# Kernel tuning notes

Measured on AMD Instinct MI355X. Metric: run time of the kernel, lower is better.

Reference implementation:

```python
import jax, jax.numpy as jnp
import numpy as np

H = 16       # num_attention_heads
KV = 4       # num_key_value_heads
HD = 128     # head_dim
BASE = 10000.0


def rotate_half(x):
    x1, x2 = jnp.split(x, 2, axis=-1)
    return jnp.concatenate((-x2, x1), axis=-1)


def rope_cos_sin(position_ids):
    # inv_freq: (HD/2,)
    inv_freq = 1.0 / (BASE ** (jnp.arange(0, HD, 2, dtype=jnp.float32) / HD))
    freqs = position_ids.astype(jnp.float32)[..., None] * inv_freq  # (B, S, HD/2)
    emb = jnp.concatenate((freqs, freqs), axis=-1)  # (B, S, HD)
    return jnp.cos(emb), jnp.sin(emb)


def setup_inputs() -> dict:
    key = jax.random.key(0)
    ks = jax.random.split(key, 5)
    B, S, D = 2, 2048, 2048
    sc = 1.0 / np.sqrt(D)
    return {
        "hidden_states": jax.random.normal(ks[0], (B, S, D), jnp.float32),
        "position_ids": jnp.broadcast_to(jnp.arange(S, dtype=jnp.int32), (B, S)),
        "wq": jax.random.normal(ks[1], (H * HD, D), jnp.float32) * sc,
        "wk": jax.random.normal(ks[2], (KV * HD, D), jnp.float32) * sc,
        "wv": jax.random.normal(ks[3], (KV * HD, D), jnp.float32) * sc,
        "wo": jax.random.normal(ks[4], (H * HD, H * HD), jnp.float32) * sc,
    }


def attention_forward(hidden_states, position_ids, wq, wk, wv, wo):
    B, S, D = hidden_states.shape
    n_rep = H // KV
    # projections -> (B, heads, S, HD)
    q = (hidden_states @ wq.T).reshape(B, S, H, HD).transpose(0, 2, 1, 3)
    k = (hidden_states @ wk.T).reshape(B, S, KV, HD).transpose(0, 2, 1, 3)
    v = (hidden_states @ wv.T).reshape(B, S, KV, HD).transpose(0, 2, 1, 3)
    # RoPE
    cos, sin = rope_cos_sin(position_ids)  # (B, S, HD)
    cos = cos[:, None]  # (B, 1, S, HD)
    sin = sin[:, None]
    q = q * cos + rotate_half(q) * sin
    k = k * cos + rotate_half(k) * sin
    # repeat kv heads for GQA: (B, KV, S, HD) -> (B, H, S, HD)
    k = jnp.repeat(k, n_rep, axis=1)
    v = jnp.repeat(v, n_rep, axis=1)
    scale = 1.0 / np.sqrt(HD)
    scores = jnp.einsum("bhqd,bhkd->bhqk", q, k) * scale
    attn = jax.nn.softmax(scores.astype(jnp.float32), axis=-1).astype(q.dtype)
    out = jnp.einsum("bhqk,bhkd->bhqd", attn, v)
    out = out.transpose(0, 2, 1, 3).reshape(B, S, H * HD)
    return out @ wo.T


def reference(hidden_states, position_ids, wq, wk, wv, wo):
    return attention_forward(hidden_states, position_ids, wq, wk, wv, wo)
```

## Files before the change

kernel.cpp:

```cpp
#include <hip/hip_runtime.h>
#include <hip/hip_bf16.h>
#include <math.h>


typedef __attribute__((ext_vector_type(4))) float f32x4;
typedef __attribute__((ext_vector_type(8))) short short8;
typedef __attribute__((ext_vector_type(4))) unsigned short u16x4;
typedef __attribute__((ext_vector_type(8))) unsigned short u16x8;

static __device__ __forceinline__ unsigned short f2bf(float x) {
    unsigned u = __builtin_bit_cast(unsigned, x);
    u += 0x7fffu + ((u >> 16) & 1u);
    return (unsigned short)(u >> 16);
}
static __device__ __forceinline__ float bf2f(unsigned short h) {
    unsigned u = ((unsigned)h) << 16;
    return __builtin_bit_cast(float, u);
}

static __device__ __forceinline__ void gload16(const unsigned short* g, unsigned short* lds) {
    __builtin_amdgcn_global_load_lds((const __attribute__((address_space(1))) void*)g,
                                     (__attribute__((address_space(3))) void*)lds, 16, 0, 0);
}

__global__ __launch_bounds__(256) void k_conv(const float* __restrict__ src,
                                              unsigned short* __restrict__ dst, int n4) {
    int i = blockIdx.x * 256 + threadIdx.x;
    if (i >= n4) return;
    f32x4 v = ((const f32x4*)src)[i];
    u16x4 o;
    o.x = f2bf(v.x); o.y = f2bf(v.y); o.z = f2bf(v.z); o.w = f2bf(v.w);
    ((u16x4*)dst)[i] = o;
}

__global__ __launch_bounds__(256) void k_conv_wqkv(const float* __restrict__ wq,
                                                   const float* __restrict__ wk,
                                                   const float* __restrict__ wv,
                                                   unsigned short* __restrict__ dst) {
    int i = blockIdx.x * 256 + threadIdx.x;
    long flat = (long)i * 4;
    int row = (int)(flat >> 11);
    int col = (int)(flat & 2047);
    const float* src;
    if (row < 2048)      src = wq + (size_t)row * 2048;
    else if (row < 2560) src = wk + (size_t)(row - 2048) * 2048;
    else                 src = wv + (size_t)(row - 2560) * 2048;
    f32x4 v = *(const f32x4*)(src + col);
    u16x4 o;
    o.x = f2bf(v.x); o.y = f2bf(v.y); o.z = f2bf(v.z); o.w = f2bf(v.w);
    *(u16x4*)(dst + flat) = o;
}

__global__ void k_rope_table(const int* __restrict__ pos_ids, float2* __restrict__ tb) {
    int r = blockIdx.x;
    int i = threadIdx.x;
    float pos = (float)pos_ids[r];
    float powv = (float)pow(10000.0, (double)i / 64.0);
    float invf = 1.0f / powv;
    float arg  = pos * invf;
    double a = (double)arg;
    tb[(size_t)r * 64 + i] = make_float2((float)cos(a), (float)sin(a));
}

__global__ __launch_bounds__(256) void k_rope_apply(unsigned short* __restrict__ qkv,
                                                    const float2* __restrict__ tb) {
    int row = blockIdx.x;
    int tid = threadIdx.x;
    int dp = tid & 63;
    float2 cs = tb[(size_t)row * 64 + dp];
    size_t base = (size_t)row * 3072;
    const float qs = 0.08838834764831845f;
    #pragma unroll
    for (int j = tid; j < 1024; j += 256) {
        int h = j >> 6;
        size_t off = base + h * 128 + dp;
        float x0 = bf2f(qkv[off]), x1 = bf2f(qkv[off + 64]);
        qkv[off]      = f2bf((x0 * cs.x - x1 * cs.y) * qs);
        qkv[off + 64] = f2bf((x1 * cs.x + x0 * cs.y) * qs);
    }
    {
        int kv = tid >> 6;
        size_t off = base + 2048 + kv * 128 + dp;
        float x0 = bf2f(qkv[off]), x1 = bf2f(qkv[off + 64]);
        qkv[off]      = f2bf(x0 * cs.x - x1 * cs.y);
        qkv[off + 64] = f2bf(x1 * cs.x + x0 * cs.y);
    }
}

__global__ __launch_bounds__(256) void k_vtrans(const unsigned short* __restrict__ qkv,
                                                unsigned short* __restrict__ vt) {
    int idx = blockIdx.x * 256 + threadIdx.x;
    int schunk = idx & 255;
    int orow = idx >> 8;
    int d = orow & 127;
    int bkv = orow >> 7;
    int b = bkv >> 2, kv = bkv & 3;
    const unsigned short* src = qkv + (size_t)(b * 2048 + schunk * 8) * 3072 + 2560 + kv * 128 + d;
    u16x8 v;
    #pragma unroll
    for (int j = 0; j < 8; ++j) v[j] = src[(size_t)j * 3072];
    *(u16x8*)(vt + (size_t)orow * 2048 + schunk * 8) = v;
}

template <int OUTF32>
__global__ __launch_bounds__(256) void k_gemm_bt(const unsigned short* __restrict__ A,
                                                 const unsigned short* __restrict__ W,
                                                 void* __restrict__ Cout,
                                                 int M, int N, int K) {
    __shared__ unsigned short As[4096];
    __shared__ unsigned short Ws[4096];
    const int tid = threadIdx.x;
    const int lane = tid & 63;
    const int w = tid >> 6;
    const int q = lane & 15, g = lane >> 4;
    const int wr = w >> 1, wc = w & 1;
    const long mbase = (long)blockIdx.y * 128;
    const long nbase = (long)blockIdx.x * 128;

    const unsigned short* gA[2];
    const unsigned short* gW[2];
    #pragma unroll
    for (int j = 0; j < 2; ++j) {
        int r = j * 64 + (tid >> 2);
        int slot = (tid & 3) ^ ((r >> 1) & 3);
        gA[j] = A + (size_t)(mbase + r) * K + slot * 8;
        gW[j] = W + (size_t)(nbase + r) * K + slot * 8;
    }
    const int sa = (g ^ ((q >> 1) & 3)) * 8;

    f32x4 acc[4][4];
    #pragma unroll
    for (int m = 0; m < 4; ++m)
        #pragma unroll
        for (int n = 0; n < 4; ++n) acc[m][n] = (f32x4){0.f, 0.f, 0.f, 0.f};

    for (int kk = 0; kk < K; kk += 32) {
        __syncthreads();
        #pragma unroll
        for (int j = 0; j < 2; ++j) {
            gload16(gA[j], &As[j * 2048 + w * 512]);
            gload16(gW[j], &Ws[j * 2048 + w * 512]);
            gA[j] += 32; gW[j] += 32;
        }
        __syncthreads();
        short8 af[4], bfr[4];
        #pragma unroll
        for (int m = 0; m < 4; ++m) af[m] = *(const short8*)&As[(wr * 64 + m * 16 + q) * 32 + sa];
        #pragma unroll
        for (int n = 0; n < 4; ++n) bfr[n] = *(const short8*)&Ws[(wc * 64 + n * 16 + q) * 32 + sa];
        #pragma unroll
        for (int m = 0; m < 4; ++m)
            #pragma unroll
            for (int n = 0; n < 4; ++n)
                acc[m][n] = __builtin_amdgcn_mfma_f32_16x16x32_bf16(af[m], bfr[n], acc[m][n], 0, 0, 0);
    }

    #pragma unroll
    for (int m = 0; m < 4; ++m)
        #pragma unroll
        for (int n = 0; n < 4; ++n)
            #pragma unroll
            for (int rr = 0; rr < 4; ++rr) {
                long row = mbase + wr * 64 + m * 16 + 4 * g + rr;
                long col = nbase + wc * 64 + n * 16 + q;
                if (OUTF32) ((float*)Cout)[row * N + col] = acc[m][n][rr];
                else ((unsigned short*)Cout)[row * N + col] = f2bf(acc[m][n][rr]);
            }
}

__global__ __launch_bounds__(256, 2) void k_flash(const unsigned short* __restrict__ qkv,
                                                  const unsigned short* __restrict__ vt,
                                                  unsigned short* __restrict__ aout) {
    __shared__ unsigned short Ks[2][8192];
    __shared__ unsigned short Vs[2][8192];
    __shared__ unsigned short Plds[4][1152];
    const int wg = blockIdx.x;
    const int kvg = wg & 7;
    const int inner = wg >> 3;
    const int h_in = inner & 3;
    const int qt = inner >> 2;
    const int b = kvg >> 2, kvh = kvg & 3;
    const int h = kvh * 4 + h_in;
    const int tid = threadIdx.x;
    const int w = tid >> 6, lane = tid & 63;
    const int q = lane & 15, g = lane >> 4;
    const int qrow = qt * 128 + w * 32;

    short8 qf[2][4];
    #pragma unroll
    for (int u = 0; u < 2; ++u) {
        const unsigned short* Qp = qkv + (size_t)(b * 2048 + qrow + u * 16 + q) * 3072 + h * 128 + g * 8;
        #pragma unroll
        for (int t = 0; t < 4; ++t) qf[u][t] = *(const short8*)(Qp + t * 32);
    }

    const unsigned short* Kbase = qkv + (size_t)(b * 2048) * 3072 + 2048 + kvh * 128;
    const unsigned short* Vbase = vt + (size_t)((b * 4 + kvh) * 128) * 2048;
    const unsigned short* gK[4];
    const unsigned short* gV[4];
    #pragma unroll
    for (int i = 0; i < 4; ++i) {
        int rowK = w * 16 + i * 4 + (lane >> 4);
        gK[i] = Kbase + (size_t)rowK * 3072 + (((lane & 15) ^ (rowK & 7)) << 3);
        int rowV = w * 32 + i * 8 + (lane >> 3);
        gV[i] = Vbase + (size_t)rowV * 2048 + (((lane & 7) ^ (rowV & 7)) << 3);
    }

    const int swz = (q & 7) << 3;
    int tcK[4];
    #pragma unroll
    for (int t = 0; t < 4; ++t) tcK[t] = (t * 32 + g * 8) ^ swz;

    unsigned short* Pw = Plds[w];

    float m_run[2] = {-INFINITY, -INFINITY};
    float l_run[2] = {0.f, 0.f};
    f32x4 o[2][8];
    #pragma unroll
    for (int u = 0; u < 2; ++u)
        #pragma unroll
        for (int nf = 0; nf < 8; ++nf) o[u][nf] = (f32x4){0.f, 0.f, 0.f, 0.f};

    auto STAGE = [&](int buf) {
        #pragma unroll
        for (int i = 0; i < 4; ++i) {
            gload16(gK[i], &Ks[buf][w * 2048 + i * 512]);
            gload16(gV[i], &Vs[buf][w * 2048 + i * 512]);
            gK[i] += 64 * 3072;
            gV[i] += 64;
        }
    };

    STAGE(0);
    int cur = 0;
    for (int t0 = 0; t0 < 32; ++t0) {
        if (t0 > 0) __builtin_amdgcn_s_barrier();
        if (t0 + 1 < 32) {
            STAGE(cur ^ 1);
            asm volatile("s_waitcnt vmcnt(8)" ::: "memory");
        } else {
            asm volatile("s_waitcnt vmcnt(0)" ::: "memory");
        }
        __builtin_amdgcn_s_barrier();

        const unsigned short* Kt = Ks[cur];
        const unsigned short* Vt = Vs[cur];

        f32x4 st[2][4];
        #pragma unroll
        for (int ks = 0; ks < 4; ++ks) {
            f32x4 a0 = (f32x4){0.f, 0.f, 0.f, 0.f};
            f32x4 a1 = (f32x4){0.f, 0.f, 0.f, 0.f};
            int rb = (ks * 16 + q) * 128;
            #pragma unroll
            for (int t = 0; t < 4; ++t) {
                short8 kf = *(const short8*)&Kt[rb + tcK[t]];
                a0 = __builtin_amdgcn_mfma_f32_16x16x32_bf16(kf, qf[0][t], a0, 0, 0, 0);
                a1 = __builtin_amdgcn_mfma_f32_16x16x32_bf16(kf, qf[1][t], a1, 0, 0, 0);
            }
            st[0][ks] = a0; st[1][ks] = a1;
        }

        short8 pa[2][2];
        #pragma unroll
        for (int u = 0; u < 2; ++u) {
            float mx = -INFINITY;
            #pragma unroll
            for (int ks = 0; ks < 4; ++ks)
                #pragma unroll
                for (int rr = 0; rr < 4; ++rr) mx = fmaxf(mx, st[u][ks][rr]);
            mx = fmaxf(mx, __shfl_xor(mx, 16));
            mx = fmaxf(mx, __shfl_xor(mx, 32));
            if (__any(mx - m_run[u] > 8.0f)) {
                float mn = fmaxf(m_run[u], mx);
                float sc = __expf(m_run[u] - mn);
                l_run[u] *= sc;
                f32x4 sv;
                #pragma unroll
                for (int rr = 0; rr < 4; ++rr) sv[rr] = __shfl(sc, 4 * g + rr);
                #pragma unroll
                for (int nf = 0; nf < 8; ++nf) o[u][nf] *= sv;
                m_run[u] = mn;
            }
            float ls = 0.f;
            float p[4][4];
            #pragma unroll
            for (int ks = 0; ks < 4; ++ks)
                #pragma unroll
                for (int rr = 0; rr < 4; ++rr) {
                    float pv = __expf(st[u][ks][rr] - m_run[u]);
                    p[ks][rr] = pv; ls += pv;
                }
            ls += __shfl_xor(ls, 16);
            ls += __shfl_xor(ls, 32);
            l_run[u] += ls;

            #pragma unroll
            for (int ks = 0; ks < 4; ++ks) {
                u16x4 pk;
                #pragma unroll
                for (int rr = 0; rr < 4; ++rr) pk[rr] = f2bf(p[ks][rr]);
                *(u16x4*)&Pw[q * 72 + ks * 16 + 4 * g] = pk;
            }
            asm volatile("s_waitcnt lgkmcnt(0)" ::: "memory");
            pa[u][0] = *(const short8*)&Pw[q * 72 + g * 8];
            pa[u][1] = *(const short8*)&Pw[q * 72 + 32 + g * 8];
        }

        #pragma unroll
        for (int nf = 0; nf < 8; ++nf) {
            int rb = (nf * 16 + q) * 64;
            f32x4 b0 = o[0][nf], b1 = o[1][nf];
            #pragma unroll
            for (int t = 0; t < 2; ++t) {
                short8 vf = *(const short8*)&Vt[rb + tcK[t]];
                b0 = __builtin_amdgcn_mfma_f32_16x16x32_bf16(pa[0][t], vf, b0, 0, 0, 0);
                b1 = __builtin_amdgcn_mfma_f32_16x16x32_bf16(pa[1][t], vf, b1, 0, 0, 0);
            }
            o[0][nf] = b0; o[1][nf] = b1;
        }
        cur ^= 1;
    }

    #pragma unroll
    for (int u = 0; u < 2; ++u) {
        f32x4 li;
        #pragma unroll
        for (int rr = 0; rr < 4; ++rr) li[rr] = __shfl(l_run[u], 4 * g + rr);
        #pragma unroll
        for (int nf = 0; nf < 8; ++nf)
            #pragma unroll
            for (int rr = 0; rr < 4; ++rr) {
                size_t row = (size_t)(b * 2048 + qrow + u * 16 + 4 * g + rr);
                aout[row * 2048 + h * 128 + nf * 16 + q] = f2bf(o[u][nf][rr] / li[rr]);
            }
    }
}

extern "C" void kernel_launch(void* const* d_in, const int* in_sizes, int n_in,
                              void* d_out, int out_size, void* d_ws, size_t ws_size,
                              hipStream_t stream) {
    (void)in_sizes; (void)n_in; (void)out_size; (void)ws_size;
    const float* hs = (const float*)d_in[0];
    const int* pos  = (const int*)d_in[1];
    const float* wq = (const float*)d_in[2];
    const float* wk = (const float*)d_in[3];
    const float* wv = (const float*)d_in[4];
    const float* wo = (const float*)d_in[5];
    float* out = (float*)d_out;

    unsigned short* hsb   = (unsigned short*)d_ws;
    unsigned short* wqkvb = hsb + (size_t)4096 * 2048;
    unsigned short* wob   = wqkvb + (size_t)3072 * 2048;
    unsigned short* qkvt  = wob + (size_t)2048 * 2048;
    unsigned short* vtb   = qkvt + (size_t)4096 * 3072;
    float2* tb            = (float2*)(vtb + (size_t)8 * 128 * 2048);
    unsigned short* aoutb = (unsigned short*)(tb + (size_t)4096 * 64);

    k_conv<<<8192, 256, 0, stream>>>(hs, hsb, 2097152);
    k_conv_wqkv<<<6144, 256, 0, stream>>>(wq, wk, wv, wqkvb);
    k_conv<<<4096, 256, 0, stream>>>(wo, wob, 1048576);
    k_rope_table<<<4096, 64, 0, stream>>>(pos, tb);
    k_gemm_bt<0><<<dim3(24, 32), 256, 0, stream>>>(hsb, wqkvb, (void*)qkvt, 4096, 3072, 2048);
    k_rope_apply<<<4096, 256, 0, stream>>>(qkvt, tb);
    k_vtrans<<<1024, 256, 0, stream>>>(qkvt, vtb);
    k_flash<<<dim3(512), 256, 0, stream>>>(qkvt, vtb, aoutb);
    k_gemm_bt<1><<<dim3(16, 32), 256, 0, stream>>>(aoutb, wob, (void*)out, 4096, 2048, 2048);
}
```

Before: 258.7 us.

## Fuse RoPE and V transpose into QKV GEMM epilogue, double-buffer GEMM, use exp2

The Q and K weight rows are permuted at conversion time so that each RoPE pair lands in adjacent output columns. That lets the QKV GEMM epilogue apply RoPE with a lane shuffle, fold in the softmax scale times log2(e), and write V straight into transposed layout. This removes the separate rope_apply and vtrans kernels and their extra passes over the QKV buffer. The GEMM main loop gains LDS double buffering with explicit vmcnt waits. The flash kernel switches from __expf to raw v_exp_f32 and preloads the V fragments before the softmax; this raises register pressure and moves work into a more complex epilogue with strided stores.

```diff
diff --git a/kernel.cpp b/kernel.cpp
--- a/kernel.cpp
+++ b/kernel.cpp
@@ -17,7 +17,11 @@
     unsigned u = ((unsigned)h) << 16;
     return __builtin_bit_cast(float, u);
 }
-
+static __device__ __forceinline__ float exp2_fast(float x) {
+    float r;
+    asm volatile("v_exp_f32 %0, %1" : "=v"(r) : "v"(x));
+    return r;
+}
 static __device__ __forceinline__ void gload16(const unsigned short* g, unsigned short* lds) {
     __builtin_amdgcn_global_load_lds((const __attribute__((address_space(1))) void*)g,
                                      (__attribute__((address_space(3))) void*)lds, 16, 0, 0);
@@ -42,9 +46,14 @@
     int row = (int)(flat >> 11);
     int col = (int)(flat & 2047);
     const float* src;
-    if (row < 2048)      src = wq + (size_t)row * 2048;
-    else if (row < 2560) src = wk + (size_t)(row - 2048) * 2048;
-    else                 src = wv + (size_t)(row - 2560) * 2048;
+    if (row < 2560) {
+        int base = row & 2047;
+        int hh = base >> 7, ii = base & 127;
+        int d = (ii >> 1) + ((ii & 1) << 6);
+        src = (row < 2048 ? wq : wk) + (size_t)(hh * 128 + d) * 2048;
+    } else {
+        src = wv + (size_t)(row - 2560) * 2048;
+    }
     f32x4 v = *(const f32x4*)(src + col);
     u16x4 o;
     o.x = f2bf(v.x); o.y = f2bf(v.y); o.z = f2bf(v.z); o.w = f2bf(v.w);
@@ -62,53 +71,16 @@
     tb[(size_t)r * 64 + i] = make_float2((float)cos(a), (float)sin(a));
 }
 
-__global__ __launch_bounds__(256) void k_rope_apply(unsigned short* __restrict__ qkv,
-                                                    const float2* __restrict__ tb) {
-    int row = blockIdx.x;
-    int tid = threadIdx.x;
-    int dp = tid & 63;
-    float2 cs = tb[(size_t)row * 64 + dp];
-    size_t base = (size_t)row * 3072;
-    const float qs = 0.08838834764831845f;
-    #pragma unroll
-    for (int j = tid; j < 1024; j += 256) {
-        int h = j >> 6;
-        size_t off = base + h * 128 + dp;
-        float x0 = bf2f(qkv[off]), x1 = bf2f(qkv[off + 64]);
-        qkv[off]      = f2bf((x0 * cs.x - x1 * cs.y) * qs);
-        qkv[off + 64] = f2bf((x1 * cs.x + x0 * cs.y) * qs);
-    }
-    {
-        int kv = tid >> 6;
-        size_t off = base + 2048 + kv * 128 + dp;
-        float x0 = bf2f(qkv[off]), x1 = bf2f(qkv[off + 64]);
-        qkv[off]      = f2bf(x0 * cs.x - x1 * cs.y);
-        qkv[off + 64] = f2bf(x1 * cs.x + x0 * cs.y);
-    }
-}
-
-__global__ __launch_bounds__(256) void k_vtrans(const unsigned short* __restrict__ qkv,
-                                                unsigned short* __restrict__ vt) {
-    int idx = blockIdx.x * 256 + threadIdx.x;
-    int schunk = idx & 255;
-    int orow = idx >> 8;
-    int d = orow & 127;
-    int bkv = orow >> 7;
-    int b = bkv >> 2, kv = bkv & 3;
-    const unsigned short* src = qkv + (size_t)(b * 2048 + schunk * 8) * 3072 + 2560 + kv * 128 + d;
-    u16x8 v;
-    #pragma unroll
-    for (int j = 0; j < 8; ++j) v[j] = src[(size_t)j * 3072];
-    *(u16x8*)(vt + (size_t)orow * 2048 + schunk * 8) = v;
-}
-
-template <int OUTF32>
-__global__ __launch_bounds__(256) void k_gemm_bt(const unsigned short* __restrict__ A,
-                                                 const unsigned short* __restrict__ W,
-                                                 void* __restrict__ Cout,
-                                                 int M, int N, int K) {
-    __shared__ unsigned short As[4096];
-    __shared__ unsigned short Ws[4096];
+template <int EPI>
+__global__ __launch_bounds__(256) void k_gemm(const unsigned short* __restrict__ A,
+                                              const unsigned short* __restrict__ W,
+                                              float* __restrict__ Cf,
+                                              unsigned short* __restrict__ qkvt,
+                                              unsigned short* __restrict__ vtb,
+                                              const float2* __restrict__ tb,
+                                              int M, int N, int K) {
+    __shared__ unsigned short As[2][4096];
+    __shared__ unsigned short Ws[2][4096];
     const int tid = threadIdx.x;
     const int lane = tid & 63;
     const int w = tid >> 6;
@@ -134,38 +106,91 @@
         #pragma unroll
         for (int n = 0; n < 4; ++n) acc[m][n] = (f32x4){0.f, 0.f, 0.f, 0.f};
 
-    for (int kk = 0; kk < K; kk += 32) {
-        __syncthreads();
+    auto STAGE = [&](int buf) {
         #pragma unroll
         for (int j = 0; j < 2; ++j) {
-            gload16(gA[j], &As[j * 2048 + w * 512]);
-            gload16(gW[j], &Ws[j * 2048 + w * 512]);
+            gload16(gA[j], &As[buf][j * 2048 + w * 512]);
+            gload16(gW[j], &Ws[buf][j * 2048 + w * 512]);
             gA[j] += 32; gW[j] += 32;
         }
-        __syncthreads();
+    };
+
+    const int nk = K >> 5;
+    STAGE(0);
+    int cur = 0;
+    for (int t = 0; t < nk; ++t) {
+        if (t) __builtin_amdgcn_s_barrier();
+        if (t + 1 < nk) {
+            STAGE(cur ^ 1);
+            asm volatile("s_waitcnt vmcnt(4)" ::: "memory");
+        } else {
+            asm volatile("s_waitcnt vmcnt(0)" ::: "memory");
+        }
+        __builtin_amdgcn_s_barrier();
+
         short8 af[4], bfr[4];
         #pragma unroll
-        for (int m = 0; m < 4; ++m) af[m] = *(const short8*)&As[(wr * 64 + m * 16 + q) * 32 + sa];
-        #pragma unroll
-        for (int n = 0; n < 4; ++n) bfr[n] = *(const short8*)&Ws[(wc * 64 + n * 16 + q) * 32 + sa];
+        for (int m = 0; m < 4; ++m) af[m] = *(const short8*)&As[cur][(wr * 64 + m * 16 + q) * 32 + sa];
+        #pragma unroll
+        for (int n = 0; n < 4; ++n) bfr[n] = *(const short8*)&Ws[cur][(wc * 64 + n * 16 + q) * 32 + sa];
         #pragma unroll
         for (int m = 0; m < 4; ++m)
             #pragma unroll
             for (int n = 0; n < 4; ++n)
                 acc[m][n] = __builtin_amdgcn_mfma_f32_16x16x32_bf16(af[m], bfr[n], acc[m][n], 0, 0, 0);
-    }
-
-    #pragma unroll
-    for (int m = 0; m < 4; ++m)
-        #pragma unroll
-        for (int n = 0; n < 4; ++n)
-            #pragma unroll
-            for (int rr = 0; rr < 4; ++rr) {
-                long row = mbase + wr * 64 + m * 16 + 4 * g + rr;
-                long col = nbase + wc * 64 + n * 16 + q;
-                if (OUTF32) ((float*)Cout)[row * N + col] = acc[m][n][rr];
-                else ((unsigned short*)Cout)[row * N + col] = f2bf(acc[m][n][rr]);
-            }
+        cur ^= 1;
+    }
+
+    if (EPI == 0) {
+        #pragma unroll
+        for (int m = 0; m < 4; ++m)
+            #pragma unroll
+            for (int n = 0; n < 4; ++n)
+                #pragma unroll
+                for (int rr = 0; rr < 4; ++rr) {
+                    long row = mbase + wr * 64 + m * 16 + 4 * g + rr;
+                    long col = nbase + wc * 64 + n * 16 + q;
+                    Cf[row * N + col] = acc[m][n][rr];
+                }
+    } else {
+        const int tile = blockIdx.x;
+        if (tile >= 20) {
+            const int kv = tile - 20;
+            #pragma unroll
+            for (int m = 0; m < 4; ++m)
+                #pragma unroll
+                for (int n = 0; n < 4; ++n) {
+                    int c = wc * 64 + n * 16 + q;
+                    long r0 = mbase + wr * 64 + m * 16 + 4 * g;
+                    int b = (int)(r0 >> 11), s0 = (int)(r0 & 2047);
+                    u16x4 pk;
+                    #pragma unroll
+                    for (int rr = 0; rr < 4; ++rr) pk[rr] = f2bf(acc[m][n][rr]);
+                    *(u16x4*)(vtb + (size_t)((b * 4 + kv) * 128 + c) * 2048 + s0) = pk;
+                }
+        } else {
+            const float scale = (tile < 16) ? 0.12751744f : 1.0f;
+            const float sgn = (q & 1) ? 1.f : -1.f;
+            #pragma unroll
+            for (int m = 0; m < 4; ++m)
+                #pragma unroll
+                for (int rr = 0; rr < 4; ++rr) {
+                    long row = mbase + wr * 64 + m * 16 + 4 * g + rr;
+                    #pragma unroll
+                    for (int n = 0; n < 4; ++n) {
+                        int c = wc * 64 + n * 16 + q;
+                        float x = acc[m][n][rr];
+                        float p = __shfl_xor(x, 1);
+                        float2 cs = tb[row * 64 + (c >> 1)];
+                        float y = (x * cs.x + sgn * (p * cs.y)) * scale;
+                        int dorig = (c >> 1) + ((c & 1) << 6);
+                        long col = (tile < 16) ? (tile * 128 + dorig)
+                                               : (2048 + (tile - 16) * 128 + dorig);
+                        qkvt[row * 3072 + col] = f2bf(y);
+                    }
+                }
+        }
+    }
 }
 
 __global__ __launch_bounds__(256, 2) void k_flash(const unsigned short* __restrict__ qkv,
@@ -261,19 +286,26 @@
             st[0][ks] = a0; st[1][ks] = a1;
         }
 
-        short8 pa[2][2];
+        short8 vf[8][2];
+        #pragma unroll
+        for (int nf = 0; nf < 8; ++nf) {
+            int rb = (nf * 16 + q) * 64;
+            #pragma unroll
+            for (int t = 0; t < 2; ++t) vf[nf][t] = *(const short8*)&Vt[rb + tcK[t]];
+        }
+
         #pragma unroll
         for (int u = 0; u < 2; ++u) {
-            float mx = -INFINITY;
-            #pragma unroll
-            for (int ks = 0; ks < 4; ++ks)
-                #pragma unroll
-                for (int rr = 0; rr < 4; ++rr) mx = fmaxf(mx, st[u][ks][rr]);
+            float mx = fmaxf(
+                fmaxf(fmaxf(fmaxf(st[u][0][0], st[u][0][1]), fmaxf(st[u][0][2], st[u][0][3])),
+                      fmaxf(fmaxf(st[u][1][0], st[u][1][1]), fmaxf(st[u][1][2], st[u][1][3]))),
+                fmaxf(fmaxf(fmaxf(st[u][2][0], st[u][2][1]), fmaxf(st[u][2][2], st[u][2][3])),
+                      fmaxf(fmaxf(st[u][3][0], st[u][3][1]), fmaxf(st[u][3][2], st[u][3][3]))));
             mx = fmaxf(mx, __shfl_xor(mx, 16));
             mx = fmaxf(mx, __shfl_xor(mx, 32));
             if (__any(mx - m_run[u] > 8.0f)) {
                 float mn = fmaxf(m_run[u], mx);
-                float sc = __expf(m_run[u] - mn);
+                float sc = exp2_fast(m_run[u] - mn);
                 l_run[u] *= sc;
                 f32x4 sv;
                 #pragma unroll
@@ -282,15 +314,13 @@
                 for (int nf = 0; nf < 8; ++nf) o[u][nf] *= sv;
                 m_run[u] = mn;
             }
-            float ls = 0.f;
-            float p[4][4];
+            f32x4 pe[4];
             #pragma unroll
             for (int ks = 0; ks < 4; ++ks)
                 #pragma unroll
-                for (int rr = 0; rr < 4; ++rr) {
-                    float pv = __expf(st[u][ks][rr] - m_run[u]);
-                    p[ks][rr] = pv; ls += pv;
-                }
+                for (int rr = 0; rr < 4; ++rr) pe[ks][rr] = exp2_fast(st[u][ks][rr] - m_run[u]);
+            f32x4 ls4 = (pe[0] + pe[1]) + (pe[2] + pe[3]);
+            float ls = (ls4[0] + ls4[1]) + (ls4[2] + ls4[3]);
             ls += __shfl_xor(ls, 16);
             ls += __shfl_xor(ls, 32);
             l_run[u] += ls;
@@ -299,25 +329,20 @@
             for (int ks = 0; ks < 4; ++ks) {
                 u16x4 pk;
                 #pragma unroll
-                for (int rr = 0; rr < 4; ++rr) pk[rr] = f2bf(p[ks][rr]);
+                for (int rr = 0; rr < 4; ++rr) pk[rr] = f2bf(pe[ks][rr]);
                 *(u16x4*)&Pw[q * 72 + ks * 16 + 4 * g] = pk;
             }
             asm volatile("s_waitcnt lgkmcnt(0)" ::: "memory");
-            pa[u][0] = *(const short8*)&Pw[q * 72 + g * 8];
-            pa[u][1] = *(const short8*)&Pw[q * 72 + 32 + g * 8];
-        }
-
-        #pragma unroll
-        for (int nf = 0; nf < 8; ++nf) {
-            int rb = (nf * 16 + q) * 64;
-            f32x4 b0 = o[0][nf], b1 = o[1][nf];
-            #pragma unroll
-            for (int t = 0; t < 2; ++t) {
-                short8 vf = *(const short8*)&Vt[rb + tcK[t]];
-                b0 = __builtin_amdgcn_mfma_f32_16x16x32_bf16(pa[0][t], vf, b0, 0, 0, 0);
-                b1 = __builtin_amdgcn_mfma_f32_16x16x32_bf16(pa[1][t], vf, b1, 0, 0, 0);
-            }
-            o[0][nf] = b0; o[1][nf] = b1;
+            short8 pa0 = *(const short8*)&Pw[q * 72 + g * 8];
+            short8 pa1 = *(const short8*)&Pw[q * 72 + 32 + g * 8];
+
+            #pragma unroll
+            for (int nf = 0; nf < 8; ++nf) {
+                f32x4 a = o[u][nf];
+                a = __builtin_amdgcn_mfma_f32_16x16x32_bf16(pa0, vf[nf][0], a, 0, 0, 0);
+                a = __builtin_amdgcn_mfma_f32_16x16x32_bf16(pa1, vf[nf][1], a, 0, 0, 0);
+                o[u][nf] = a;
+            }
         }
         cur ^= 1;
     }
@@ -361,9 +386,7 @@
     k_conv_wqkv<<<6144, 256, 0, stream>>>(wq, wk, wv, wqkvb);
     k_conv<<<4096, 256, 0, stream>>>(wo, wob, 1048576);
     k_rope_table<<<4096, 64, 0, stream>>>(pos, tb);
-    k_gemm_bt<0><<<dim3(24, 32), 256, 0, stream>>>(hsb, wqkvb, (void*)qkvt, 4096, 3072, 2048);
-    k_rope_apply<<<4096, 256, 0, stream>>>(qkvt, tb);
-    k_vtrans<<<1024, 256, 0, stream>>>(qkvt, vtb);
+    k_gemm<1><<<dim3(24, 32), 256, 0, stream>>>(hsb, wqkvb, nullptr, qkvt, vtb, tb, 4096, 3072, 2048);
     k_flash<<<dim3(512), 256, 0, stream>>>(qkvt, vtb, aoutb);
-    k_gemm_bt<1><<<dim3(16, 32), 256, 0, stream>>>(aoutb, wob, (void*)out, 4096, 2048, 2048);
-}
+    k_gemm<0><<<dim3(16, 32), 256, 0, stream>>>(aoutb, wob, out, nullptr, nullptr, nullptr, 4096, 2048, 2048);
+}
```

Measured after the change: 233.2 us. 9.9% less time.
